# Performance work log

Measured on AMD Instinct MI355X. Metric: run time of the kernel, lower is better.

The kernel has to match this reference:

```python
import jax, jax.numpy as jnp
import numpy as np

BINS = 2048
DST_NBINS = 8
STEP = 1e-5


def _get_norm(delta_begin, delta_end, density):
    # integral of x^2 * density over [delta_begin, delta_end]
    return density * (delta_end ** 3 - delta_begin ** 3) / 3.0


def _quant_error(hist, bin_width, nsb, neb):
    # L2 quantization error of mapping src bins [nsb, neb] onto DST_NBINS bins
    dst_w = bin_width * (neb - nsb + 1).astype(jnp.float32) / DST_NBINS
    safe_w = jnp.where(dst_w == 0.0, 1.0, dst_w)
    src = jnp.arange(BINS, dtype=jnp.float32)
    begin = (src - nsb) * bin_width          # src bin left edge rel. to new range
    end = begin + bin_width
    db = jnp.clip(jnp.floor(begin / safe_w), 0, DST_NBINS - 1)
    de = jnp.clip(jnp.floor(end / safe_w), 0, DST_NBINS - 1)
    density = hist / bin_width
    db_c = (db + 0.5) * safe_w
    norm = _get_norm(begin - db_c, safe_w / 2, density)
    norm = norm + (de - db - 1.0) * _get_norm(-safe_w / 2, safe_w / 2, density)
    de_c = de * safe_w + safe_w / 2
    norm = norm + _get_norm(-safe_w / 2, end - de_c, density)
    return jnp.where(dst_w == 0.0, jnp.float32(0.0), norm.sum())


def _search(hist, min_val, max_val):
    # entropy-style greedy shrink of [start_bin, end_bin]; sequential, data-dependent
    bin_width = (max_val - min_val) / BINS
    total = hist.sum()
    cSum = jnp.cumsum(hist)

    def cond(s):
        alpha, beta, sb, eb, nm, done = s
        return (alpha < beta) & jnp.logical_not(done)

    def body(s):
        alpha, beta, sb, eb, nm, done = s
        na = alpha + STEP
        nb = beta - STEP
        # l: first bin (>= sb) with cSum >= na*total; r: last bin with cSum <= nb*total
        l = jnp.clip(jnp.searchsorted(cSum, na * total, side='left'), sb, eb)
        r = jnp.clip(jnp.searchsorted(cSum, nb * total, side='right') - 1, sb, eb)
        take_left = (l - sb) > (eb - r)
        nsb = jnp.where(take_left, l, sb)
        neb = jnp.where(take_left, eb, r)
        alpha2 = jnp.where(take_left, na, alpha)
        beta2 = jnp.where(take_left, beta, nb)
        changed = (nsb != sb) | (neb != eb)
        norm = _quant_error(hist, bin_width, nsb, neb)
        broke = changed & (norm > nm)
        accept = changed & jnp.logical_not(broke)
        return (alpha2, beta2,
                jnp.where(accept, nsb, sb),
                jnp.where(accept, neb, eb),
                jnp.where(accept, norm, nm),
                done | broke)

    init = (jnp.float32(0.0), jnp.float32(1.0),
            jnp.int32(0), jnp.int32(BINS - 1),
            jnp.float32(jnp.inf), jnp.bool_(False))
    _, _, sb, eb, _, _ = jax.lax.while_loop(cond, body, init)
    return sb, eb


def _forward(x):
    min_val = jnp.min(x)
    max_val = jnp.max(x)
    bin_width = (max_val - min_val) / BINS
    safe_bw = jnp.where(bin_width == 0.0, 1.0, bin_width)
    # torch.histc equivalent over [min_val, max_val]
    idx = jnp.clip(jnp.floor((x.ravel() - min_val) / safe_bw).astype(jnp.int32), 0, BINS - 1)
    hist = jnp.zeros(BINS, jnp.float32).at[idx].add(1.0)
    sb, eb = _search(jax.lax.stop_gradient(hist),
                     jax.lax.stop_gradient(min_val),
                     jax.lax.stop_gradient(max_val))
    new_min = min_val + bin_width * sb
    new_max = min_val + bin_width * (eb + 1)
    return jnp.stack([new_min, new_max])


def setup_inputs() -> dict:
    key = jax.random.key(0)
    x = jax.random.normal(key, (32, 1024, 1024), dtype=jnp.float32)
    return {"x": x}


def reference(x):
    return _forward(x)
```

## Files before the change

### kernel.cpp

```cpp
#include <hip/hip_runtime.h>
#include <float.h>
#include <math.h>

#define BINS 2048
#define DSTN 8
#define STEPF 1e-5f
#define NPART 1024
#define MAXST 2048
#define NSEG 64
#define MINF 0x7fffffff
#define NT 512

struct Ws {
  float pmin[NPART];
  float pmax[NPART];
  float min_val, max_val, bin_width, safe_bw;
  int   n_states;
  int   pad[3];
  unsigned int hist[BINS];
  float histf[BINS];
  float norms[MAXST];
  int2  states[MAXST];
};

__global__ void __launch_bounds__(256) k_minmax(const float* __restrict__ x, long long n,
                                                Ws* __restrict__ ws) {
  long long n4 = n >> 2;
  float vmin = FLT_MAX, vmax = -FLT_MAX;
  const float4* __restrict__ x4 = (const float4*)x;
  long long stride = (long long)gridDim.x * blockDim.x;
  for (long long i = (long long)blockIdx.x * blockDim.x + threadIdx.x; i < n4; i += stride) {
    float4 v = x4[i];
    vmin = fminf(vmin, fminf(fminf(v.x, v.y), fminf(v.z, v.w)));
    vmax = fmaxf(vmax, fmaxf(fmaxf(v.x, v.y), fmaxf(v.z, v.w)));
  }
  for (long long i = (n4 << 2) + (long long)blockIdx.x * blockDim.x + threadIdx.x; i < n; i += stride) {
    float v = x[i];
    vmin = fminf(vmin, v); vmax = fmaxf(vmax, v);
  }
  for (int off = 32; off > 0; off >>= 1) {
    vmin = fminf(vmin, __shfl_down(vmin, off));
    vmax = fmaxf(vmax, __shfl_down(vmax, off));
  }
  __shared__ float smin[4], smax[4];
  int wid = threadIdx.x >> 6;
  if ((threadIdx.x & 63) == 0) { smin[wid] = vmin; smax[wid] = vmax; }
  __syncthreads();
  if (threadIdx.x == 0) {
    float a = smin[0], b = smax[0];
    int nw = (int)(blockDim.x >> 6);
    for (int w = 1; w < nw; ++w) { a = fminf(a, smin[w]); b = fmaxf(b, smax[w]); }
    ws->pmin[blockIdx.x] = a; ws->pmax[blockIdx.x] = b;
  }
}

__global__ void __launch_bounds__(256) k_minmax_final(Ws* __restrict__ ws, int nparts) {
  __shared__ float smin[256], smax[256];
  int t = threadIdx.x;
  float vmin = FLT_MAX, vmax = -FLT_MAX;
  for (int i = t; i < nparts; i += 256) {
    vmin = fminf(vmin, ws->pmin[i]);
    vmax = fmaxf(vmax, ws->pmax[i]);
  }
  smin[t] = vmin; smax[t] = vmax;
  __syncthreads();
  for (int off = 128; off > 0; off >>= 1) {
    if (t < off) { smin[t] = fminf(smin[t], smin[t + off]); smax[t] = fmaxf(smax[t], smax[t + off]); }
    __syncthreads();
  }
  if (t == 0) {
    float mn = smin[0], mx = smax[0];
    ws->min_val = mn; ws->max_val = mx;
    float bw = (mx - mn) / (float)BINS;
    ws->bin_width = bw;
    ws->safe_bw = (bw == 0.0f) ? 1.0f : bw;
  }
  for (int i = t; i < BINS; i += 256) ws->hist[i] = 0u;
}

__global__ void __launch_bounds__(256) k_hist(const float* __restrict__ x, long long n,
                                              Ws* __restrict__ ws) {
  __shared__ __align__(16) unsigned int lh[BINS * 4];
  for (int i = threadIdx.x; i < BINS * 4; i += 256) lh[i] = 0u;
  __syncthreads();
  float minv = ws->min_val;
  float sbw = ws->safe_bw;
  int sub = threadIdx.x & 3;
  long long n4 = n >> 2;
  const float4* __restrict__ x4 = (const float4*)x;
  long long stride = (long long)gridDim.x * blockDim.x;
  for (long long i = (long long)blockIdx.x * blockDim.x + threadIdx.x; i < n4; i += stride) {
    float4 v = x4[i];
    int a = (int)floorf((v.x - minv) / sbw);
    int b = (int)floorf((v.y - minv) / sbw);
    int c = (int)floorf((v.z - minv) / sbw);
    int d = (int)floorf((v.w - minv) / sbw);
    a = min(BINS - 1, max(0, a));
    b = min(BINS - 1, max(0, b));
    c = min(BINS - 1, max(0, c));
    d = min(BINS - 1, max(0, d));
    atomicAdd(&lh[(a << 2) | sub], 1u);
    atomicAdd(&lh[(b << 2) | sub], 1u);
    atomicAdd(&lh[(c << 2) | sub], 1u);
    atomicAdd(&lh[(d << 2) | sub], 1u);
  }
  for (long long i = (n4 << 2) + (long long)blockIdx.x * blockDim.x + threadIdx.x; i < n; i += stride) {
    int a = (int)floorf((x[i] - minv) / sbw);
    a = min(BINS - 1, max(0, a));
    atomicAdd(&lh[(a << 2) | sub], 1u);
  }
  __syncthreads();
  for (int i = threadIdx.x; i < BINS; i += 256) {
    uint4 v = *((const uint4*)lh + i);
    unsigned int c = v.x + v.y + v.z + v.w;
    if (c) atomicAdd(&ws->hist[i], c);
  }
}

__global__ void __launch_bounds__(NT) k_search(Ws* __restrict__ ws) {
  __shared__ __align__(16) char arena[49216];
  float* csum   = (float*)(arena);
  float* Atab   = (float*)(arena + 8192);
  int2*  ev     = (int2*)(arena);
  int2*  ltmt   = (int2*)(arena + 16400);
  int*   mcross = (int*)(arena + 32816);
  int*   chain  = (int*)(arena + 41008);
  __shared__ __align__(16) int2 sstates[MAXST];
  __shared__ float fred[8];
  __shared__ int   ired[8], ired2[8];
  __shared__ __align__(16) int4 segB4[NSEG];
  __shared__ __align__(16) int4 segA4[NSEG];
  __shared__ int segklo[NSEG], segblo[NSEG];
  __shared__ int nseg_s, mbot_s, nsegA_s, nc_s;
  __shared__ int pub_mode, pub_j0, pub_sb, pub_mt, pub_nst0, pub_nfire, pub_clamp, pub_ntot;

  int t = threadIdx.x;
  int lane = t & 63, wid = t >> 6;
  const float S = STEPF;

  float loc[4];
  float s = 0.0f;
  #pragma unroll
  for (int kk = 0; kk < 4; ++kk) {
    float h = (float)ws->hist[t * 4 + kk];
    ws->histf[t * 4 + kk] = h;
    s += h;
    loc[kk] = s;
  }
  float isc = s;
  #pragma unroll
  for (int off = 1; off < 64; off <<= 1) {
    float u = __shfl_up(isc, off);
    if (lane >= off) isc += u;
  }
  if (lane == 63) fred[wid] = isc;
  __syncthreads();
  if (t < 8) {
    float v = fred[t];
    #pragma unroll
    for (int off = 1; off < 8; off <<= 1) {
      float u = __shfl_up(v, off, 8);
      if ((t & 7) >= off) v += u;
    }
    fred[t] = v;
  }
  __syncthreads();
  {
    float base = wid ? fred[wid - 1] : 0.0f;
    float excl = base + (isc - s);
    #pragma unroll
    for (int kk = 0; kk < 4; ++kk) csum[t * 4 + kk] = excl + loc[kk];
  }
  __syncthreads();

  const float T = csum[BINS - 1];
  const float rcpT = 1.0f / T;

  if (t == 0) {
    int sg = 0; float B = 1.0f; int m0 = 0; int mbot = MINF;
    while (sg < NSEG && B > 0.0f) {
      float Bn = B - S;
      if (Bn <= 0.0f) {
        segB4[sg] = make_int4(__float_as_int(B), __float_as_int(B - Bn), m0, 0);
        ++sg; mbot = m0 + 1; break;
      }
      float d = B - Bn;
      unsigned bb = __float_as_uint(B);
      unsigned bid = bb & 0x7f800000u;
      if ((bb & 0x007fffffu) == 0u) bid -= 0x00800000u;
      float binlo = __uint_as_float(bid);
      float brel = B - binlo;
      int n = (int)floor((double)brel / (double)d);
      if (n < 0) n = 0;
      if (n >= 2) {
        float B1 = B - d;
        float B2 = B1 - S;
        if (B1 - B2 != d) n = 1;
      }
      segB4[sg] = make_int4(__float_as_int(B), __float_as_int(d), m0, n);
      ++sg;
      float Blast = B - (float)n * d;
      B = Blast - S;
      m0 += n + 1;
      if (B <= 0.0f) { mbot = m0; break; }
    }
    nseg_s = sg; mbot_s = mbot;

    int sa = 0;
    segA4[sa++] = make_int4(__float_as_int(0.0f), __float_as_int(S), 0, 0);
    float A0 = S; int k0 = 1;
    while (sa < NSEG && k0 <= 2051) {
      float An = A0 + S;
      float d = An - A0;
      unsigned ab = __float_as_uint(A0);
      unsigned abid = ab & 0x7f800000u;
      float binhi = __uint_as_float(abid + 0x00800000u);
      float brel = binhi - A0;
      int n = (int)floorf(brel / d);
      if (n < 0) n = 0;
      while (n >= 1 && !(A0 + (float)n * d < binhi)) --n;
      while (A0 + (float)(n + 1) * d < binhi) ++n;
      if (n >= 2) {
        float A1 = A0 + d;
        float A2 = A1 + S;
        if (A2 - A1 != d) n = 1;
      }
      if (k0 + n > 2051) n = 2051 - k0;
      segA4[sa++] = make_int4(__float_as_int(A0), __float_as_int(d), k0, n);
      float Alast = A0 + (float)n * d;
      A0 = Alast + S;
      k0 += n + 1;
    }
    nsegA_s = sa;
  }
  __syncthreads();

  int nsg = nseg_s;
  int mbot = mbot_s;
  int nsa = nsegA_s;

  for (int sg = 0; sg < nsa; ++sg) {
    int4 sv = segA4[sg];
    float A0v = __int_as_float(sv.x), dv = __int_as_float(sv.y);
    for (int i = t; i <= sv.w; i += NT) Atab[sv.z + i] = A0v + (float)i * dv;
  }
  __syncthreads();

  {
    int okA = 1;
    for (int k = t; k < 2051; k += NT) okA &= (Atab[k] + S == Atab[k + 1]) ? 1 : 0;
    if (__syncthreads_and(okA) == 0) {
      if (t == 0) {
        float a = 0.0f; Atab[0] = 0.0f;
        for (int k = 1; k < 2052; ++k) { a = a + S; Atab[k] = a; }
      }
      __syncthreads();
    }
  }

  {
    int lov[5], hiv[5];
    float av1[5];
    #pragma unroll
    for (int i = 0; i < 5; ++i) {
      int k = t + NT * i;
      lov[i] = 0; hiv[i] = BINS;
      av1[i] = (k <= 2050) ? Atab[k + 1] * T : FLT_MAX;
    }
    #pragma unroll
    for (int lev = 0; lev < 12; ++lev) {
      #pragma unroll
      for (int i = 0; i < 5; ++i) {
        bool act = lov[i] < hiv[i];
        int mid = act ? ((lov[i] + hiv[i]) >> 1) : 0;
        float cv = csum[mid];
        bool g = act && (cv < av1[i]);
        lov[i] = g ? (mid + 1) : lov[i];
        hiv[i] = (act && !g) ? mid : hiv[i];
      }
    }
    #pragma unroll
    for (int i = 0; i < 5; ++i) {
      int k = t + NT * i;
      if (k < 2052) ltmt[k] = make_int2((k <= 2050) ? lov[i] : BINS, 0);
    }
  }
  if (t < nsg) {
    int4 sv = segB4[t];
    float Bs = __int_as_float(sv.x), dd = __int_as_float(sv.y);
    float Bend = Bs - (float)sv.w * dd;
    int lo = 0, hi = 2052;
    while (lo < hi) { int mid = (lo + hi) >> 1; if (Atab[mid] < Bend) lo = mid + 1; else hi = mid; }
    segklo[t] = lo;
    float vt = Bend * T;
    lo = 0; hi = BINS;
    while (lo < hi) { int mid = (lo + hi) >> 1; if (!(csum[mid] > vt)) lo = mid + 1; else hi = mid; }
    segblo[t] = lo;
  }
  __syncthreads();

  {
    int* ltY = (int*)ltmt;
    for (int sg = 0; sg < nsg; ++sg) {
      int lo = segklo[sg], hi = (sg ? segklo[sg - 1] : 2052);
      if (lo >= hi) continue;
      int4 sv = segB4[sg];
      float Bs = __int_as_float(sv.x), dd = __int_as_float(sv.y);
      int ms = sv.z, n = sv.w;
      float rd = (dd > 0.0f) ? 1.0f / dd : 0.0f;
      for (int k = lo + t; k < hi; k += NT) {
        float a = Atab[k];
        int i2 = (int)((Bs - a) * rd);
        if (i2 < 0) i2 = 0; if (i2 > n) i2 = n;
        while (i2 > 0 && Bs - (float)(i2 - 1) * dd <= a) --i2;
        while (i2 <= n && Bs - (float)i2 * dd > a) ++i2;
        ltY[2 * k + 1] = ms + i2;
      }
    }
    int dhi = segklo[nsg - 1];
    for (int k = t; k < dhi; k += NT) ltY[2 * k + 1] = mbot;
  }
  {
    for (int sg = 0; sg < nsg; ++sg) {
      int lo = segblo[sg], hi = (sg ? segblo[sg - 1] : BINS);
      if (lo >= hi) continue;
      int4 sv = segB4[sg];
      float Bs = __int_as_float(sv.x), dd = __int_as_float(sv.y);
      int ms = sv.z, n = sv.w;
      float rd = (dd > 0.0f) ? 1.0f / dd : 0.0f;
      for (int b = lo + t; b < hi; b += NT) {
        float c = csum[b];
        int i2 = (int)((Bs - c * rcpT) * rd);
        if (i2 < 0) i2 = 0; if (i2 > n) i2 = n;
        while (i2 > 0 && (Bs - (float)(i2 - 1) * dd) * T < c) --i2;
        while (i2 <= n && !((Bs - (float)i2 * dd) * T < c)) ++i2;
        mcross[b] = ms + i2 - 1;
      }
    }
    int dhi = segblo[nsg - 1];
    for (int b = t; b < dhi; b += NT) {
      float c = csum[b];
      mcross[b] = (c > 0.0f) ? ((mbot == MINF) ? MINF : (mbot - 1)) : MINF;
    }
  }
  __syncthreads();

  int iem = 0, cnt = 0;
  {
    int b0 = t * 4;
    int mcl[4];
    #pragma unroll
    for (int kk = 0; kk < 4; ++kk) mcl[kk] = mcross[b0 + kk];
    int mnext = (t < NT - 1) ? mcross[b0 + 4] : 0;
    #pragma unroll
    for (int kk = 0; kk < 4; ++kk) {
      int nxtv = (kk < 3) ? mcl[kk + 1] : mnext;
      bool e = (b0 + kk == BINS - 1) || (mcl[kk] != nxtv);
      iem |= e ? (1 << kk) : 0;
      cnt += e ? 1 : 0;
    }
  }
  {
    int inc = cnt;
    #pragma unroll
    for (int off = 1; off < 64; off <<= 1) {
      int u = __shfl_up(inc, off);
      if (lane >= off) inc += u;
    }
    if (lane == 63) ired[wid] = inc;
    __syncthreads();
    if (t < 8) {
      int v = ired[t];
      #pragma unroll
      for (int off = 1; off < 8; off <<= 1) {
        int u = __shfl_up(v, off, 8);
        if ((t & 7) >= off) v += u;
      }
      ired[t] = v;
    }
    __syncthreads();
    int base = wid ? ired[wid - 1] : 0;
    int incl_t = base + inc;
    int total = ired[7];
    int running = total - incl_t;
    #pragma unroll
    for (int kk = 3; kk >= 0; --kk) {
      if (iem & (1 << kk)) { ++running; chain[running - 1] = t * 4 + kk; }
    }
    if (t == 0) nc_s = total;
  }
  __syncthreads();

  int NC = nc_s;
  for (int j = 1 + t; j <= NC; j += NT) {
    int prev = chain[j - 1];
    ev[j] = make_int2(mcross[prev], (j < NC) ? chain[j] : -1);
  }
  if (t == 0 && NC < 2048) ev[NC + 1] = make_int2(MINF, -1);
  __syncthreads();

  if (t == 0) {
    int k = 0, sb = 0, eb = BINS - 1, m = 0, j = 1, nst = 0;
    int2 lm0 = ltmt[0], lm1 = ltmt[1], lm2 = ltmt[2];
    int2 e0 = ev[1], e1 = ev[2], e2 = ev[3];
    int mode = 0;
    int guard = 0;
    pub_j0 = 0; pub_sb = 0; pub_mt = 0;
    while (++guard < 6000) {
      int lpos = lm0.x, mt = lm0.y;
      int mc = e0.x, ne = e0.y;
      int l = min(lpos, eb);
      int pl = l - sb;
      if (pl <= 0) { mode = 1; pub_j0 = j; pub_sb = sb; pub_mt = mt; break; }
      if (m >= mt) break;
      bool coin = (m == mc);
      int nec = max(ne, sb);
      int pr = eb - nec;
      bool fl = !coin || (pl > pr);
      if (fl) {
        sb = l; ++k;
        if (nst < MAXST) sstates[nst] = make_int2(sb, eb);
        ++nst;
        if (sb >= eb) break;
        lm0 = lm1; lm1 = lm2; lm2 = ltmt[min(k + 2, 2051)];
      } else {
        eb = nec; m = mc + 1; ++j;
        if (nst < MAXST) sstates[nst] = make_int2(sb, eb);
        ++nst;
        if (sb >= eb) break;
        e0 = e1; e1 = e2; e2 = ev[min(j + 2, 2048)];
      }
    }
    pub_mode = mode;
    pub_nst0 = (nst < MAXST) ? nst : MAXST;
  }
  __syncthreads();

  int mode = pub_mode;
  int nst0 = pub_nst0;
  if (mode == 1) {
    int j0 = pub_j0, sbF = pub_sb, mtF = pub_mt;
    int locA = NC + 1, locB = NC + 1;
    for (int j = j0 + t; j <= NC; j += NT) {
      int2 e = ev[j];
      if (e.x >= mtF && j < locA) locA = j;
      if (e.y <= sbF && j < locB) locB = j;
    }
    #pragma unroll
    for (int off = 32; off > 0; off >>= 1) {
      locA = min(locA, __shfl_down(locA, off));
      locB = min(locB, __shfl_down(locB, off));
    }
    if (lane == 0) { ired[wid] = locA; ired2[wid] = locB; }
    __syncthreads();
    if (t == 0) {
      int jA = NC + 1, jB = NC + 1;
      for (int w = 0; w < 8; ++w) { jA = min(jA, ired[w]); jB = min(jB, ired2[w]); }
      int nfire, clampLast;
      if (jB < jA) { nfire = jB - j0 + 1; clampLast = 1; }
      else         { nfire = jA - j0;     clampLast = 0; }
      if (nfire < 0) nfire = 0;
      int ntot = nst0 + nfire;
      if (ntot > MAXST) ntot = MAXST;
      pub_nfire = nfire; pub_clamp = clampLast; pub_ntot = ntot;
    }
    __syncthreads();
    int nfire = pub_nfire, clampLast = pub_clamp;
    for (int i = t; i < nfire; i += NT) {
      int idx = nst0 + i;
      if (idx < MAXST) {
        int y = ev[j0 + i].y;
        ws->states[idx] = make_int2(sbF, (clampLast && i == nfire - 1) ? sbF : y);
      }
    }
    if (t == 0) ws->n_states = pub_ntot;
  } else {
    if (t == 0) ws->n_states = nst0;
  }
  for (int i = t; i < nst0; i += NT) ws->states[i] = sstates[i];
}

__global__ void __launch_bounds__(256) k_eval(Ws* __restrict__ ws) {
  int i = blockIdx.x;
  if (i >= ws->n_states) return;
  int2 st = ws->states[i];
  float bw = ws->bin_width;
  float cnt = (float)(st.y - st.x + 1);
  float w = bw * cnt / (float)DSTN;
  int t = threadIdx.x;
  if (w == 0.0f) {
    if (t == 0) ws->norms[i] = 0.0f;
    return;
  }
  float hw = 0.5f * w;
  float hw3 = hw * hw * hw;
  float nsb = (float)st.x;
  float sum = 0.0f;
  #pragma unroll
  for (int k = 0; k < 8; ++k) {
    int j = t + 256 * k;
    float h = ws->histf[j];
    float begin = ((float)j - nsb) * bw;
    float end = begin + bw;
    float db = fminf(fmaxf(floorf(begin / w), 0.0f), (float)(DSTN - 1));
    float de = fminf(fmaxf(floorf(end / w), 0.0f), (float)(DSTN - 1));
    float density = h / bw;
    float dbc = (db + 0.5f) * w;
    float a1 = begin - dbc;
    float n1 = density * (hw3 - a1 * a1 * a1) / 3.0f;
    float nmid = density * (hw3 + hw3) / 3.0f;
    float dec = de * w + hw;
    float a3 = end - dec;
    float n3 = density * (a3 * a3 * a3 + hw3) / 3.0f;
    sum += n1 + (de - db - 1.0f) * nmid + n3;
  }
  __shared__ float red[256];
  red[t] = sum;
  __syncthreads();
  for (int off = 128; off > 0; off >>= 1) {
    if (t < off) red[t] += red[t + off];
    __syncthreads();
  }
  if (t == 0) ws->norms[i] = red[0];
}

__global__ void __launch_bounds__(256) k_final(Ws* __restrict__ ws, float* __restrict__ out) {
  __shared__ int sbrk[256];
  int N = ws->n_states;
  int t = threadIdx.x;
  int loc = 0x7fffffff;
  for (int i = t + 1; i < N; i += 256) {
    if (ws->norms[i] > ws->norms[i - 1]) loc = min(loc, i);
  }
  sbrk[t] = loc;
  __syncthreads();
  for (int off = 128; off > 0; off >>= 1) {
    if (t < off) sbrk[t] = min(sbrk[t], sbrk[t + off]);
    __syncthreads();
  }
  if (t == 0) {
    int sb, eb;
    if (N == 0) { sb = 0; eb = BINS - 1; }
    else {
      int ib = sbrk[0];
      int fi = (ib != 0x7fffffff) ? (ib - 1) : (N - 1);
      int2 st = ws->states[fi];
      sb = st.x; eb = st.y;
    }
    float minv = ws->min_val, bw = ws->bin_width;
    out[0] = minv + bw * (float)sb;
    out[1] = minv + bw * (float)(eb + 1);
  }
}

extern "C" void kernel_launch(void* const* d_in, const int* in_sizes, int n_in,
                              void* d_out, int out_size, void* d_ws, size_t ws_size,
                              hipStream_t stream) {
  const float* x = (const float*)d_in[0];
  long long n = (long long)in_sizes[0];
  Ws* ws = (Ws*)d_ws;
  float* out = (float*)d_out;

  k_minmax<<<NPART, 256, 0, stream>>>(x, n, ws);
  k_minmax_final<<<1, 256, 0, stream>>>(ws, NPART);
  k_hist<<<NPART, 256, 0, stream>>>(x, n, ws);
  k_search<<<1, NT, 0, stream>>>(ws);
  k_eval<<<MAXST, 256, 0, stream>>>(ws);
  k_final<<<1, 256, 0, stream>>>(ws, out);
}
```

Measured before the change: 155.3 us.

## Fuse reductions via last-block pattern and move search precompute into minmax grid

Folds the min/max final reduction into k_minmax using an atomic last-block counter, and likewise fuses the norm evaluation with the final break-point scan. An extra block in the minmax grid now builds the step tables (Atab, mterm, segment descriptors) in parallel with the data pass, taking that serial setup off the single-block search kernel. The search kernel widens to 1024 threads, writes states straight to global memory, and the histogram grid is halved. This removes two launches and serial work, in exchange for atomics and threadfences, a memset, and more global-memory traffic inside the search.

```diff
diff --git a/kernel.cpp b/kernel.cpp
--- a/kernel.cpp
+++ b/kernel.cpp
@@ -5,36 +5,162 @@
 #define BINS 2048
 #define DSTN 8
 #define STEPF 1e-5f
-#define NPART 1024
+#define NMM 1024
+#define NHIST 512
 #define MAXST 2048
 #define NSEG 64
 #define MINF 0x7fffffff
-#define NT 512
+#define NT 1024
 
 struct Ws {
-  float pmin[NPART];
-  float pmax[NPART];
+  unsigned int mm_done, ev_done;
+  int nseg, mbot;
+  int n_states;
+  int pad0[3];
   float min_val, max_val, bin_width, safe_bw;
-  int   n_states;
-  int   pad[3];
+  float pmin[NMM];
+  float pmax[NMM];
   unsigned int hist[BINS];
   float histf[BINS];
+  float Atab[2052];
+  int   mterm[2052];
+  int4  segB4[NSEG];
   float norms[MAXST];
   int2  states[MAXST];
 };
 
 __global__ void __launch_bounds__(256) k_minmax(const float* __restrict__ x, long long n,
                                                 Ws* __restrict__ ws) {
+  __shared__ float smin[4], smax[4];
+  __shared__ float redn[256], redx[256];
+  __shared__ __align__(16) int4 sB4[NSEG], sA4[NSEG];
+  __shared__ int segklo[NSEG];
+  __shared__ int s_nsg, s_mbot, s_nsa;
+  __shared__ int amLast;
+  int t = threadIdx.x;
+  const float S = STEPF;
+
+  if (blockIdx.x == NMM) {
+    if (t == 0) {
+      int sg = 0; float B = 1.0f; int m0 = 0; int mbot = MINF;
+      while (sg < NSEG && B > 0.0f) {
+        float Bn = B - S;
+        if (Bn <= 0.0f) {
+          sB4[sg] = make_int4(__float_as_int(B), __float_as_int(B - Bn), m0, 0);
+          ++sg; mbot = m0 + 1; break;
+        }
+        float d = B - Bn;
+        unsigned bb = __float_as_uint(B);
+        unsigned bid = bb & 0x7f800000u;
+        if ((bb & 0x007fffffu) == 0u) bid -= 0x00800000u;
+        float binlo = __uint_as_float(bid);
+        float brel = B - binlo;
+        int nn = (int)floor((double)brel / (double)d);
+        if (nn < 0) nn = 0;
+        if (nn >= 2) {
+          float B1 = B - d;
+          float B2 = B1 - S;
+          if (B1 - B2 != d) nn = 1;
+        }
+        sB4[sg] = make_int4(__float_as_int(B), __float_as_int(d), m0, nn);
+        ++sg;
+        float Blast = B - (float)nn * d;
+        B = Blast - S;
+        m0 += nn + 1;
+        if (B <= 0.0f) { mbot = m0; break; }
+      }
+      s_nsg = sg; s_mbot = mbot;
+      int sa = 0;
+      sA4[sa++] = make_int4(__float_as_int(0.0f), __float_as_int(S), 0, 0);
+      float A0 = S; int k0 = 1;
+      while (sa < NSEG && k0 <= 2051) {
+        float An = A0 + S;
+        float d = An - A0;
+        unsigned ab = __float_as_uint(A0);
+        unsigned abid = ab & 0x7f800000u;
+        float binhi = __uint_as_float(abid + 0x00800000u);
+        float brel = binhi - A0;
+        int nn = (int)floorf(brel / d);
+        if (nn < 0) nn = 0;
+        while (nn >= 1 && !(A0 + (float)nn * d < binhi)) --nn;
+        while (A0 + (float)(nn + 1) * d < binhi) ++nn;
+        if (nn >= 2) {
+          float A1 = A0 + d;
+          float A2 = A1 + S;
+          if (A2 - A1 != d) nn = 1;
+        }
+        if (k0 + nn > 2051) nn = 2051 - k0;
+        sA4[sa++] = make_int4(__float_as_int(A0), __float_as_int(d), k0, nn);
+        float Alast = A0 + (float)nn * d;
+        A0 = Alast + S;
+        k0 += nn + 1;
+      }
+      s_nsa = sa;
+    }
+    __syncthreads();
+    int nsg = s_nsg, mbot = s_mbot, nsa = s_nsa;
+
+    for (int sg = 0; sg < nsa; ++sg) {
+      int4 sv = sA4[sg];
+      float A0v = __int_as_float(sv.x), dv = __int_as_float(sv.y);
+      for (int i = t; i <= sv.w; i += 256) ws->Atab[sv.z + i] = A0v + (float)i * dv;
+    }
+    __syncthreads();
+    {
+      int okA = 1;
+      for (int k = t; k < 2051; k += 256) okA &= (ws->Atab[k] + S == ws->Atab[k + 1]) ? 1 : 0;
+      if (__syncthreads_and(okA) == 0) {
+        if (t == 0) {
+          float a = 0.0f; ws->Atab[0] = 0.0f;
+          for (int k = 1; k < 2052; ++k) { a = a + S; ws->Atab[k] = a; }
+        }
+        __syncthreads();
+      }
+    }
+    if (t < nsg) {
+      int4 sv = sB4[t];
+      float Bs = __int_as_float(sv.x), dd = __int_as_float(sv.y);
+      float Bend = Bs - (float)sv.w * dd;
+      int lo = 0, hi = 2052;
+      while (lo < hi) { int mid = (lo + hi) >> 1; if (ws->Atab[mid] < Bend) lo = mid + 1; else hi = mid; }
+      segklo[t] = lo;
+      ws->segB4[t] = sv;
+    }
+    if (t == 0) { ws->nseg = nsg; ws->mbot = mbot; }
+    __syncthreads();
+    for (int sg = 0; sg < nsg; ++sg) {
+      int lo = segklo[sg], hi = (sg ? segklo[sg - 1] : 2052);
+      if (lo >= hi) continue;
+      int4 sv = sB4[sg];
+      float Bs = __int_as_float(sv.x), dd = __int_as_float(sv.y);
+      int ms = sv.z, nn = sv.w;
+      float rd = (dd > 0.0f) ? 1.0f / dd : 0.0f;
+      for (int k = lo + t; k < hi; k += 256) {
+        float a = ws->Atab[k];
+        int i2 = (int)((Bs - a) * rd);
+        if (i2 < 0) i2 = 0; if (i2 > nn) i2 = nn;
+        while (i2 > 0 && Bs - (float)(i2 - 1) * dd <= a) --i2;
+        while (i2 <= nn && Bs - (float)i2 * dd > a) ++i2;
+        ws->mterm[k] = ms + i2;
+      }
+    }
+    {
+      int dhi = segklo[nsg - 1];
+      for (int k = t; k < dhi; k += 256) ws->mterm[k] = mbot;
+    }
+    return;
+  }
+
   long long n4 = n >> 2;
   float vmin = FLT_MAX, vmax = -FLT_MAX;
   const float4* __restrict__ x4 = (const float4*)x;
-  long long stride = (long long)gridDim.x * blockDim.x;
-  for (long long i = (long long)blockIdx.x * blockDim.x + threadIdx.x; i < n4; i += stride) {
+  long long stride = (long long)NMM * blockDim.x;
+  for (long long i = (long long)blockIdx.x * blockDim.x + t; i < n4; i += stride) {
     float4 v = x4[i];
     vmin = fminf(vmin, fminf(fminf(v.x, v.y), fminf(v.z, v.w)));
     vmax = fmaxf(vmax, fmaxf(fmaxf(v.x, v.y), fmaxf(v.z, v.w)));
   }
-  for (long long i = (n4 << 2) + (long long)blockIdx.x * blockDim.x + threadIdx.x; i < n; i += stride) {
+  for (long long i = (n4 << 2) + (long long)blockIdx.x * blockDim.x + t; i < n; i += stride) {
     float v = x[i];
     vmin = fminf(vmin, v); vmax = fmaxf(vmax, v);
   }
@@ -42,40 +168,39 @@
     vmin = fminf(vmin, __shfl_down(vmin, off));
     vmax = fmaxf(vmax, __shfl_down(vmax, off));
   }
-  __shared__ float smin[4], smax[4];
-  int wid = threadIdx.x >> 6;
-  if ((threadIdx.x & 63) == 0) { smin[wid] = vmin; smax[wid] = vmax; }
-  __syncthreads();
-  if (threadIdx.x == 0) {
+  int wid = t >> 6;
+  if ((t & 63) == 0) { smin[wid] = vmin; smax[wid] = vmax; }
+  __syncthreads();
+  if (t == 0) {
     float a = smin[0], b = smax[0];
-    int nw = (int)(blockDim.x >> 6);
-    for (int w = 1; w < nw; ++w) { a = fminf(a, smin[w]); b = fmaxf(b, smax[w]); }
+    for (int w = 1; w < 4; ++w) { a = fminf(a, smin[w]); b = fmaxf(b, smax[w]); }
     ws->pmin[blockIdx.x] = a; ws->pmax[blockIdx.x] = b;
-  }
-}
-
-__global__ void __launch_bounds__(256) k_minmax_final(Ws* __restrict__ ws, int nparts) {
-  __shared__ float smin[256], smax[256];
-  int t = threadIdx.x;
-  float vmin = FLT_MAX, vmax = -FLT_MAX;
-  for (int i = t; i < nparts; i += 256) {
-    vmin = fminf(vmin, ws->pmin[i]);
-    vmax = fmaxf(vmax, ws->pmax[i]);
-  }
-  smin[t] = vmin; smax[t] = vmax;
-  __syncthreads();
-  for (int off = 128; off > 0; off >>= 1) {
-    if (t < off) { smin[t] = fminf(smin[t], smin[t + off]); smax[t] = fmaxf(smax[t], smax[t + off]); }
-    __syncthreads();
-  }
-  if (t == 0) {
-    float mn = smin[0], mx = smax[0];
-    ws->min_val = mn; ws->max_val = mx;
-    float bw = (mx - mn) / (float)BINS;
-    ws->bin_width = bw;
-    ws->safe_bw = (bw == 0.0f) ? 1.0f : bw;
-  }
-  for (int i = t; i < BINS; i += 256) ws->hist[i] = 0u;
+    __threadfence();
+    amLast = (atomicAdd(&ws->mm_done, 1u) == (unsigned)(NMM - 1)) ? 1 : 0;
+  }
+  __syncthreads();
+  if (amLast) {
+    __threadfence();
+    float fmn = FLT_MAX, fmx = -FLT_MAX;
+    for (int i = t; i < NMM; i += 256) {
+      fmn = fminf(fmn, ws->pmin[i]);
+      fmx = fmaxf(fmx, ws->pmax[i]);
+    }
+    redn[t] = fmn; redx[t] = fmx;
+    __syncthreads();
+    for (int off = 128; off > 0; off >>= 1) {
+      if (t < off) { redn[t] = fminf(redn[t], redn[t + off]); redx[t] = fmaxf(redx[t], redx[t + off]); }
+      __syncthreads();
+    }
+    if (t == 0) {
+      float mn = redn[0], mx = redx[0];
+      ws->min_val = mn; ws->max_val = mx;
+      float bw = (mx - mn) / (float)BINS;
+      ws->bin_width = bw;
+      ws->safe_bw = (bw == 0.0f) ? 1.0f : bw;
+    }
+    for (int i = t; i < BINS; i += 256) ws->hist[i] = 0u;
+  }
 }
 
 __global__ void __launch_bounds__(256) k_hist(const float* __restrict__ x, long long n,
@@ -118,159 +243,72 @@
 }
 
 __global__ void __launch_bounds__(NT) k_search(Ws* __restrict__ ws) {
-  __shared__ __align__(16) char arena[49216];
-  float* csum   = (float*)(arena);
-  float* Atab   = (float*)(arena + 8192);
-  int2*  ev     = (int2*)(arena);
-  int2*  ltmt   = (int2*)(arena + 16400);
-  int*   mcross = (int*)(arena + 32816);
-  int*   chain  = (int*)(arena + 41008);
-  __shared__ __align__(16) int2 sstates[MAXST];
-  __shared__ float fred[8];
-  __shared__ int   ired[8], ired2[8];
-  __shared__ __align__(16) int4 segB4[NSEG];
-  __shared__ __align__(16) int4 segA4[NSEG];
-  __shared__ int segklo[NSEG], segblo[NSEG];
-  __shared__ int nseg_s, mbot_s, nsegA_s, nc_s;
-  __shared__ int pub_mode, pub_j0, pub_sb, pub_mt, pub_nst0, pub_nfire, pub_clamp, pub_ntot;
+  __shared__ __align__(16) float csum[BINS];
+  __shared__ __align__(16) int2  ltmt[2052];
+  __shared__ __align__(16) int   mcross[BINS];
+  __shared__ __align__(16) int   chain[2052];
+  __shared__ __align__(16) int2  ev[2049];
+  __shared__ __align__(16) int4  sB4[NSEG];
+  __shared__ int   segblo[NSEG];
+  __shared__ float fwav[16];
+  __shared__ int   ired[16], ired2[16];
+  __shared__ int   pub_nc;
+  __shared__ int   pub_mode, pub_j0, pub_sb, pub_mt, pub_nst0, pub_nfire, pub_clamp, pub_ntot;
 
   int t = threadIdx.x;
   int lane = t & 63, wid = t >> 6;
-  const float S = STEPF;
-
-  float loc[4];
-  float s = 0.0f;
-  #pragma unroll
-  for (int kk = 0; kk < 4; ++kk) {
-    float h = (float)ws->hist[t * 4 + kk];
-    ws->histf[t * 4 + kk] = h;
-    s += h;
-    loc[kk] = s;
-  }
+
+  if (t < NSEG) sB4[t] = ws->segB4[t];
+  int nsg = ws->nseg;
+  int mbot = ws->mbot;
+
+  float h0 = (float)ws->hist[2 * t];
+  float h1 = (float)ws->hist[2 * t + 1];
+  ws->histf[2 * t] = h0; ws->histf[2 * t + 1] = h1;
+  float s = h0 + h1;
   float isc = s;
   #pragma unroll
   for (int off = 1; off < 64; off <<= 1) {
     float u = __shfl_up(isc, off);
     if (lane >= off) isc += u;
   }
-  if (lane == 63) fred[wid] = isc;
-  __syncthreads();
-  if (t < 8) {
-    float v = fred[t];
+  if (lane == 63) fwav[wid] = isc;
+  __syncthreads();
+  if (t < 16) {
+    float v = fwav[t];
     #pragma unroll
-    for (int off = 1; off < 8; off <<= 1) {
-      float u = __shfl_up(v, off, 8);
-      if ((t & 7) >= off) v += u;
-    }
-    fred[t] = v;
+    for (int off = 1; off < 16; off <<= 1) {
+      float u = __shfl_up(v, off, 16);
+      if ((t & 15) >= off) v += u;
+    }
+    fwav[t] = v;
   }
   __syncthreads();
   {
-    float base = wid ? fred[wid - 1] : 0.0f;
+    float base = wid ? fwav[wid - 1] : 0.0f;
     float excl = base + (isc - s);
-    #pragma unroll
-    for (int kk = 0; kk < 4; ++kk) csum[t * 4 + kk] = excl + loc[kk];
+    csum[2 * t] = excl + h0;
+    csum[2 * t + 1] = excl + s;
   }
   __syncthreads();
 
   const float T = csum[BINS - 1];
   const float rcpT = 1.0f / T;
 
-  if (t == 0) {
-    int sg = 0; float B = 1.0f; int m0 = 0; int mbot = MINF;
-    while (sg < NSEG && B > 0.0f) {
-      float Bn = B - S;
-      if (Bn <= 0.0f) {
-        segB4[sg] = make_int4(__float_as_int(B), __float_as_int(B - Bn), m0, 0);
-        ++sg; mbot = m0 + 1; break;
-      }
-      float d = B - Bn;
-      unsigned bb = __float_as_uint(B);
-      unsigned bid = bb & 0x7f800000u;
-      if ((bb & 0x007fffffu) == 0u) bid -= 0x00800000u;
-      float binlo = __uint_as_float(bid);
-      float brel = B - binlo;
-      int n = (int)floor((double)brel / (double)d);
-      if (n < 0) n = 0;
-      if (n >= 2) {
-        float B1 = B - d;
-        float B2 = B1 - S;
-        if (B1 - B2 != d) n = 1;
-      }
-      segB4[sg] = make_int4(__float_as_int(B), __float_as_int(d), m0, n);
-      ++sg;
-      float Blast = B - (float)n * d;
-      B = Blast - S;
-      m0 += n + 1;
-      if (B <= 0.0f) { mbot = m0; break; }
-    }
-    nseg_s = sg; mbot_s = mbot;
-
-    int sa = 0;
-    segA4[sa++] = make_int4(__float_as_int(0.0f), __float_as_int(S), 0, 0);
-    float A0 = S; int k0 = 1;
-    while (sa < NSEG && k0 <= 2051) {
-      float An = A0 + S;
-      float d = An - A0;
-      unsigned ab = __float_as_uint(A0);
-      unsigned abid = ab & 0x7f800000u;
-      float binhi = __uint_as_float(abid + 0x00800000u);
-      float brel = binhi - A0;
-      int n = (int)floorf(brel / d);
-      if (n < 0) n = 0;
-      while (n >= 1 && !(A0 + (float)n * d < binhi)) --n;
-      while (A0 + (float)(n + 1) * d < binhi) ++n;
-      if (n >= 2) {
-        float A1 = A0 + d;
-        float A2 = A1 + S;
-        if (A2 - A1 != d) n = 1;
-      }
-      if (k0 + n > 2051) n = 2051 - k0;
-      segA4[sa++] = make_int4(__float_as_int(A0), __float_as_int(d), k0, n);
-      float Alast = A0 + (float)n * d;
-      A0 = Alast + S;
-      k0 += n + 1;
-    }
-    nsegA_s = sa;
-  }
-  __syncthreads();
-
-  int nsg = nseg_s;
-  int mbot = mbot_s;
-  int nsa = nsegA_s;
-
-  for (int sg = 0; sg < nsa; ++sg) {
-    int4 sv = segA4[sg];
-    float A0v = __int_as_float(sv.x), dv = __int_as_float(sv.y);
-    for (int i = t; i <= sv.w; i += NT) Atab[sv.z + i] = A0v + (float)i * dv;
-  }
-  __syncthreads();
-
   {
-    int okA = 1;
-    for (int k = t; k < 2051; k += NT) okA &= (Atab[k] + S == Atab[k + 1]) ? 1 : 0;
-    if (__syncthreads_and(okA) == 0) {
-      if (t == 0) {
-        float a = 0.0f; Atab[0] = 0.0f;
-        for (int k = 1; k < 2052; ++k) { a = a + S; Atab[k] = a; }
-      }
-      __syncthreads();
-    }
-  }
-
-  {
-    int lov[5], hiv[5];
-    float av1[5];
+    int lov[3], hiv[3];
+    float av1[3];
     #pragma unroll
-    for (int i = 0; i < 5; ++i) {
+    for (int i = 0; i < 3; ++i) {
       int k = t + NT * i;
-      lov[i] = 0; hiv[i] = BINS;
-      av1[i] = (k <= 2050) ? Atab[k + 1] * T : FLT_MAX;
+      bool has = (k <= 2050);
+      lov[i] = 0; hiv[i] = has ? BINS : 0;
+      av1[i] = has ? ws->Atab[k + 1] * T : 0.0f;
     }
     #pragma unroll
     for (int lev = 0; lev < 12; ++lev) {
       #pragma unroll
-      for (int i = 0; i < 5; ++i) {
+      for (int i = 0; i < 3; ++i) {
         bool act = lov[i] < hiv[i];
         int mid = act ? ((lov[i] + hiv[i]) >> 1) : 0;
         float cv = csum[mid];
@@ -280,63 +318,39 @@
       }
     }
     #pragma unroll
-    for (int i = 0; i < 5; ++i) {
+    for (int i = 0; i < 3; ++i) {
       int k = t + NT * i;
-      if (k < 2052) ltmt[k] = make_int2((k <= 2050) ? lov[i] : BINS, 0);
+      if (k < 2052) ltmt[k] = make_int2((k <= 2050) ? lov[i] : BINS, ws->mterm[k]);
     }
   }
   if (t < nsg) {
-    int4 sv = segB4[t];
+    int4 sv = sB4[t];
     float Bs = __int_as_float(sv.x), dd = __int_as_float(sv.y);
     float Bend = Bs - (float)sv.w * dd;
-    int lo = 0, hi = 2052;
-    while (lo < hi) { int mid = (lo + hi) >> 1; if (Atab[mid] < Bend) lo = mid + 1; else hi = mid; }
-    segklo[t] = lo;
     float vt = Bend * T;
-    lo = 0; hi = BINS;
+    int lo = 0, hi = BINS;
     while (lo < hi) { int mid = (lo + hi) >> 1; if (!(csum[mid] > vt)) lo = mid + 1; else hi = mid; }
     segblo[t] = lo;
   }
   __syncthreads();
 
+  for (int sg = 0; sg < nsg; ++sg) {
+    int lo = segblo[sg], hi = (sg ? segblo[sg - 1] : BINS);
+    if (lo >= hi) continue;
+    int4 sv = sB4[sg];
+    float Bs = __int_as_float(sv.x), dd = __int_as_float(sv.y);
+    int ms = sv.z, nn = sv.w;
+    float rd = (dd > 0.0f) ? 1.0f / dd : 0.0f;
+    for (int b = lo + t; b < hi; b += NT) {
+      float c = csum[b];
+      int i2 = (int)((Bs - c * rcpT) * rd);
+      if (i2 < 0) i2 = 0; if (i2 > nn) i2 = nn;
+      while (i2 > 0 && (Bs - (float)(i2 - 1) * dd) * T < c) --i2;
+      while (i2 <= nn && !((Bs - (float)i2 * dd) * T < c)) ++i2;
+      mcross[b] = ms + i2 - 1;
+    }
+  }
   {
-    int* ltY = (int*)ltmt;
-    for (int sg = 0; sg < nsg; ++sg) {
-      int lo = segklo[sg], hi = (sg ? segklo[sg - 1] : 2052);
-      if (lo >= hi) continue;
-      int4 sv = segB4[sg];
-      float Bs = __int_as_float(sv.x), dd = __int_as_float(sv.y);
-      int ms = sv.z, n = sv.w;
-      float rd = (dd > 0.0f) ? 1.0f / dd : 0.0f;
-      for (int k = lo + t; k < hi; k += NT) {
-        float a = Atab[k];
-        int i2 = (int)((Bs - a) * rd);
-        if (i2 < 0) i2 = 0; if (i2 > n) i2 = n;
-        while (i2 > 0 && Bs - (float)(i2 - 1) * dd <= a) --i2;
-        while (i2 <= n && Bs - (float)i2 * dd > a) ++i2;
-        ltY[2 * k + 1] = ms + i2;
-      }
-    }
-    int dhi = segklo[nsg - 1];
-    for (int k = t; k < dhi; k += NT) ltY[2 * k + 1] = mbot;
-  }
-  {
-    for (int sg = 0; sg < nsg; ++sg) {
-      int lo = segblo[sg], hi = (sg ? segblo[sg - 1] : BINS);
-      if (lo >= hi) continue;
-      int4 sv = segB4[sg];
-      float Bs = __int_as_float(sv.x), dd = __int_as_float(sv.y);
-      int ms = sv.z, n = sv.w;
-      float rd = (dd > 0.0f) ? 1.0f / dd : 0.0f;
-      for (int b = lo + t; b < hi; b += NT) {
-        float c = csum[b];
-        int i2 = (int)((Bs - c * rcpT) * rd);
-        if (i2 < 0) i2 = 0; if (i2 > n) i2 = n;
-        while (i2 > 0 && (Bs - (float)(i2 - 1) * dd) * T < c) --i2;
-        while (i2 <= n && !((Bs - (float)i2 * dd) * T < c)) ++i2;
-        mcross[b] = ms + i2 - 1;
-      }
-    }
     int dhi = segblo[nsg - 1];
     for (int b = t; b < dhi; b += NT) {
       float c = csum[b];
@@ -345,22 +359,13 @@
   }
   __syncthreads();
 
-  int iem = 0, cnt = 0;
   {
-    int b0 = t * 4;
-    int mcl[4];
-    #pragma unroll
-    for (int kk = 0; kk < 4; ++kk) mcl[kk] = mcross[b0 + kk];
-    int mnext = (t < NT - 1) ? mcross[b0 + 4] : 0;
-    #pragma unroll
-    for (int kk = 0; kk < 4; ++kk) {
-      int nxtv = (kk < 3) ? mcl[kk + 1] : mnext;
-      bool e = (b0 + kk == BINS - 1) || (mcl[kk] != nxtv);
-      iem |= e ? (1 << kk) : 0;
-      cnt += e ? 1 : 0;
-    }
-  }
-  {
+    int b0 = 2 * t;
+    int m0v = mcross[b0], m1v = mcross[b0 + 1];
+    int mnext = (t < NT - 1) ? mcross[b0 + 2] : 0;
+    bool e0b = (m0v != m1v);
+    bool e1b = (b0 + 1 == BINS - 1) || (m1v != mnext);
+    int cnt = (e0b ? 1 : 0) + (e1b ? 1 : 0);
     int inc = cnt;
     #pragma unroll
     for (int off = 1; off < 64; off <<= 1) {
@@ -369,32 +374,29 @@
     }
     if (lane == 63) ired[wid] = inc;
     __syncthreads();
-    if (t < 8) {
+    if (t < 16) {
       int v = ired[t];
       #pragma unroll
-      for (int off = 1; off < 8; off <<= 1) {
-        int u = __shfl_up(v, off, 8);
-        if ((t & 7) >= off) v += u;
+      for (int off = 1; off < 16; off <<= 1) {
+        int u = __shfl_up(v, off, 16);
+        if ((t & 15) >= off) v += u;
       }
       ired[t] = v;
     }
     __syncthreads();
     int base = wid ? ired[wid - 1] : 0;
     int incl_t = base + inc;
-    int total = ired[7];
+    int total = ired[15];
     int running = total - incl_t;
-    #pragma unroll
-    for (int kk = 3; kk >= 0; --kk) {
-      if (iem & (1 << kk)) { ++running; chain[running - 1] = t * 4 + kk; }
-    }
-    if (t == 0) nc_s = total;
-  }
-  __syncthreads();
-
-  int NC = nc_s;
+    if (e1b) { ++running; chain[running - 1] = b0 + 1; }
+    if (e0b) { ++running; chain[running - 1] = b0; }
+    if (t == 0) pub_nc = total;
+  }
+  __syncthreads();
+
+  int NC = pub_nc;
   for (int j = 1 + t; j <= NC; j += NT) {
-    int prev = chain[j - 1];
-    ev[j] = make_int2(mcross[prev], (j < NC) ? chain[j] : -1);
+    ev[j] = make_int2(mcross[chain[j - 1]], (j < NC) ? chain[j] : -1);
   }
   if (t == 0 && NC < 2048) ev[NC + 1] = make_int2(MINF, -1);
   __syncthreads();
@@ -419,13 +421,13 @@
       bool fl = !coin || (pl > pr);
       if (fl) {
         sb = l; ++k;
-        if (nst < MAXST) sstates[nst] = make_int2(sb, eb);
+        if (nst < MAXST) ws->states[nst] = make_int2(sb, eb);
         ++nst;
         if (sb >= eb) break;
         lm0 = lm1; lm1 = lm2; lm2 = ltmt[min(k + 2, 2051)];
       } else {
         eb = nec; m = mc + 1; ++j;
-        if (nst < MAXST) sstates[nst] = make_int2(sb, eb);
+        if (nst < MAXST) ws->states[nst] = make_int2(sb, eb);
         ++nst;
         if (sb >= eb) break;
         e0 = e1; e1 = e2; e2 = ev[min(j + 2, 2048)];
@@ -455,7 +457,7 @@
     __syncthreads();
     if (t == 0) {
       int jA = NC + 1, jB = NC + 1;
-      for (int w = 0; w < 8; ++w) { jA = min(jA, ired[w]); jB = min(jB, ired2[w]); }
+      for (int w = 0; w < 16; ++w) { jA = min(jA, ired[w]); jB = min(jB, ired2[w]); }
       int nfire, clampLast;
       if (jB < jA) { nfire = jB - j0 + 1; clampLast = 1; }
       else         { nfire = jA - j0;     clampLast = 0; }
@@ -477,60 +479,65 @@
   } else {
     if (t == 0) ws->n_states = nst0;
   }
-  for (int i = t; i < nst0; i += NT) ws->states[i] = sstates[i];
 }
 
-__global__ void __launch_bounds__(256) k_eval(Ws* __restrict__ ws) {
+__global__ void __launch_bounds__(256) k_evalfinal(Ws* __restrict__ ws, float* __restrict__ out) {
+  __shared__ float red[256];
+  __shared__ int sbrk[256];
+  __shared__ int amLast;
   int i = blockIdx.x;
-  if (i >= ws->n_states) return;
-  int2 st = ws->states[i];
-  float bw = ws->bin_width;
-  float cnt = (float)(st.y - st.x + 1);
-  float w = bw * cnt / (float)DSTN;
   int t = threadIdx.x;
-  if (w == 0.0f) {
-    if (t == 0) ws->norms[i] = 0.0f;
-    return;
-  }
-  float hw = 0.5f * w;
-  float hw3 = hw * hw * hw;
-  float nsb = (float)st.x;
-  float sum = 0.0f;
-  #pragma unroll
-  for (int k = 0; k < 8; ++k) {
-    int j = t + 256 * k;
-    float h = ws->histf[j];
-    float begin = ((float)j - nsb) * bw;
-    float end = begin + bw;
-    float db = fminf(fmaxf(floorf(begin / w), 0.0f), (float)(DSTN - 1));
-    float de = fminf(fmaxf(floorf(end / w), 0.0f), (float)(DSTN - 1));
-    float density = h / bw;
-    float dbc = (db + 0.5f) * w;
-    float a1 = begin - dbc;
-    float n1 = density * (hw3 - a1 * a1 * a1) / 3.0f;
-    float nmid = density * (hw3 + hw3) / 3.0f;
-    float dec = de * w + hw;
-    float a3 = end - dec;
-    float n3 = density * (a3 * a3 * a3 + hw3) / 3.0f;
-    sum += n1 + (de - db - 1.0f) * nmid + n3;
-  }
-  __shared__ float red[256];
-  red[t] = sum;
-  __syncthreads();
-  for (int off = 128; off > 0; off >>= 1) {
-    if (t < off) red[t] += red[t + off];
-    __syncthreads();
-  }
-  if (t == 0) ws->norms[i] = red[0];
-}
-
-__global__ void __launch_bounds__(256) k_final(Ws* __restrict__ ws, float* __restrict__ out) {
-  __shared__ int sbrk[256];
   int N = ws->n_states;
-  int t = threadIdx.x;
-  int loc = 0x7fffffff;
-  for (int i = t + 1; i < N; i += 256) {
-    if (ws->norms[i] > ws->norms[i - 1]) loc = min(loc, i);
+
+  if (i < N) {
+    int2 st = ws->states[i];
+    float bw = ws->bin_width;
+    float cntf = (float)(st.y - st.x + 1);
+    float w = bw * cntf / (float)DSTN;
+    if (w == 0.0f) {
+      if (t == 0) ws->norms[i] = 0.0f;
+    } else {
+      float hw = 0.5f * w;
+      float hw3 = hw * hw * hw;
+      float nsb = (float)st.x;
+      float sum = 0.0f;
+      #pragma unroll
+      for (int k = 0; k < 8; ++k) {
+        int j = t + 256 * k;
+        float h = ws->histf[j];
+        float begin = ((float)j - nsb) * bw;
+        float end = begin + bw;
+        float db = fminf(fmaxf(floorf(begin / w), 0.0f), (float)(DSTN - 1));
+        float de = fminf(fmaxf(floorf(end / w), 0.0f), (float)(DSTN - 1));
+        float density = h / bw;
+        float dbc = (db + 0.5f) * w;
+        float a1 = begin - dbc;
+        float n1 = density * (hw3 - a1 * a1 * a1) / 3.0f;
+        float nmid = density * (hw3 + hw3) / 3.0f;
+        float dec = de * w + hw;
+        float a3 = end - dec;
+        float n3 = density * (a3 * a3 * a3 + hw3) / 3.0f;
+        sum += n1 + (de - db - 1.0f) * nmid + n3;
+      }
+      red[t] = sum;
+      __syncthreads();
+      for (int off = 128; off > 0; off >>= 1) {
+        if (t < off) red[t] += red[t + off];
+        __syncthreads();
+      }
+      if (t == 0) ws->norms[i] = red[0];
+    }
+  }
+
+  __threadfence();
+  if (t == 0) amLast = (atomicAdd(&ws->ev_done, 1u) == (unsigned)(gridDim.x - 1)) ? 1 : 0;
+  __syncthreads();
+  if (!amLast) return;
+  __threadfence();
+
+  int loc = MINF;
+  for (int q = t + 1; q < N; q += 256) {
+    if (ws->norms[q] > ws->norms[q - 1]) loc = min(loc, q);
   }
   sbrk[t] = loc;
   __syncthreads();
@@ -543,7 +550,7 @@
     if (N == 0) { sb = 0; eb = BINS - 1; }
     else {
       int ib = sbrk[0];
-      int fi = (ib != 0x7fffffff) ? (ib - 1) : (N - 1);
+      int fi = (ib != MINF) ? (ib - 1) : (N - 1);
       int2 st = ws->states[fi];
       sb = st.x; eb = st.y;
     }
@@ -561,10 +568,9 @@
   Ws* ws = (Ws*)d_ws;
   float* out = (float*)d_out;
 
-  k_minmax<<<NPART, 256, 0, stream>>>(x, n, ws);
-  k_minmax_final<<<1, 256, 0, stream>>>(ws, NPART);
-  k_hist<<<NPART, 256, 0, stream>>>(x, n, ws);
+  hipMemsetAsync(d_ws, 0, 8, stream);
+  k_minmax<<<NMM + 1, 256, 0, stream>>>(x, n, ws);
+  k_hist<<<NHIST, 256, 0, stream>>>(x, n, ws);
   k_search<<<1, NT, 0, stream>>>(ws);
-  k_eval<<<MAXST, 256, 0, stream>>>(ws);
-  k_final<<<1, 256, 0, stream>>>(ws, out);
+  k_evalfinal<<<MAXST, 256, 0, stream>>>(ws, out);
 }
```

After: 278.4 us. +79.2%, slower.
